# Kernel tuning notes

Measured on AMD Instinct MI355X. Metric: run time of the kernel, lower is better.

## Reference

```python
import jax, jax.numpy as jnp
import numpy as np
import math

DIM = 1024
D_FF = 1024
B = 128


def setup_inputs() -> dict:
    key = jax.random.key(0)
    ks = jax.random.split(key, 13)
    s = 1.0 / math.sqrt(DIM)
    sf = 1.0 / math.sqrt(D_FF)
    return {
        "x": jax.random.normal(ks[0], (B, DIM), dtype=jnp.float32),
        "Wq": jax.random.uniform(ks[1], (DIM, DIM), jnp.float32, -s, s),
        "bq": jax.random.uniform(ks[2], (DIM,), jnp.float32, -s, s),
        "Wk": jax.random.uniform(ks[3], (DIM, DIM), jnp.float32, -s, s),
        "bk": jax.random.uniform(ks[4], (DIM,), jnp.float32, -s, s),
        "Wv": jax.random.uniform(ks[5], (DIM, DIM), jnp.float32, -s, s),
        "bv": jax.random.uniform(ks[6], (DIM,), jnp.float32, -s, s),
        "Wo": jax.random.uniform(ks[7], (DIM, DIM), jnp.float32, -s, s),
        "bo": jax.random.uniform(ks[8], (DIM,), jnp.float32, -s, s),
        "W1": jax.random.uniform(ks[9], (D_FF, DIM), jnp.float32, -s, s),
        "b1": jax.random.uniform(ks[10], (D_FF,), jnp.float32, -s, s),
        "W2": jax.random.uniform(ks[11], (DIM, D_FF), jnp.float32, -sf, sf),
        "b2": jax.random.uniform(ks[12], (DIM,), jnp.float32, -sf, sf),
    }


def reference(x, Wq, bq, Wk, bk, Wv, bv, Wo, bo, W1, b1, W2, b2):
    # Attention (eval mode: dropout is identity)
    q = x @ Wq.T + bq                      # [B, D]
    k = x @ Wk.T + bk                      # [B, D]
    v = x @ Wv.T + bv                      # [B, D]
    inv_sqrt_dk = 1.0 / math.sqrt(DIM)
    # per-sample outer product: weights[b, i, j] = q[b,i] * k[b,j] / sqrt(d_k)
    weights = (q[:, :, None] * k[:, None, :]) * inv_sqrt_dk  # [B, D, D]
    nw = jax.nn.softmax(weights, axis=-1)                    # [B, D, D]
    attn_out = jnp.einsum('bij,bj->bi', nw, v)               # [B, D]
    attn_out = attn_out @ Wo.T + bo
    # residual 1
    x2 = x + attn_out
    # FFN
    h = jax.nn.relu(x2 @ W1.T + b1)        # [B, d_ff]
    ff = h @ W2.T + b2                     # [B, D]
    out = x2 + ff
    return (out, nw)
```

## Files before the change

kernel.cpp:

```cpp
#include <hip/hip_runtime.h>

#define DIM   1024
#define BATCH 128
#define MAT   (BATCH*DIM)
#define NROWS MAT
#define DS    32

typedef float f4n __attribute__((ext_vector_type(4)));

#define A1_R0 0
#define A1_N  26624
#define B1_R0 26624
#define B1_N  17408
#define A2_R0 44032
#define A2_N  26624
#define B2_R0 70656
#define B2_N  17408
#define A3_R0 88064
#define A3_N  26624
#define B3_R0 114688
#define B3_N  16384

struct Params {
  const float *x,*Wq,*bq,*Wk,*bk,*Wv,*bv,*Wo,*bo,*W1,*b1,*W2,*b2;
  float *out,*nw;
  float *q,*k,*v,*araw,*x2,*h,*rinv,*P;
};

__device__ __forceinline__ void fill_write(const Params& p, int T, int NT,
                                           int row0, int nrows)
{
  const size_t base = (size_t)row0 << 8;
  const size_t end  = base + ((size_t)nrows << 8);
  f4n* __restrict__ nw4 = (f4n*)p.nw;
#pragma unroll 2
  for (size_t f = base + T; f < end; f += NT) {
    const int row = (int)(f >> 8);
    const int c4  = (int)(f & 255);
    const int b   = row >> 10;
    const f4n kk = *(const f4n*)(p.k + ((size_t)b<<10) + (c4<<2));
    const float c    = p.q[row] * 0.03125f;
    const float rinv = p.rinv[row];
    f4n st;
    st.x=__expf(c*kk.x)*rinv; st.y=__expf(c*kk.y)*rinv;
    st.z=__expf(c*kk.z)*rinv; st.w=__expf(c*kk.w)*rinv;
    nw4[f] = st;
  }
}

__device__ __forceinline__ void gemm_tile(
    const float* __restrict__ X, const float* __restrict__ W,
    float* __restrict__ Pout, int n0, int k0, int KC,
    float* xt, float* wt)
{
  const int tid = threadIdx.x;
  const int tn = tid & 15, tb = tid >> 4;
  const int b_base = tb*8, n_base = tn*4;
  float acc[8][4];
#pragma unroll
  for (int i=0;i<8;++i)
#pragma unroll
    for (int j=0;j<4;++j) acc[i][j]=0.f;

  for (int s=0; s<KC/DS; ++s) {
    const int kk = k0 + s*DS;
#pragma unroll
    for (int r=0;r<4;++r) {
      const int row = (tid>>3) + 32*r;
      const int c0  = (tid&7)*4;
      const float4 vv = *(const float4*)(X + (size_t)row*DIM + kk + c0);
      xt[(c0+0)*132+row]=vv.x; xt[(c0+1)*132+row]=vv.y;
      xt[(c0+2)*132+row]=vv.z; xt[(c0+3)*132+row]=vv.w;
    }
#pragma unroll
    for (int r=0;r<2;++r) {
      const int row = (tid>>3) + 32*r;
      const int c0  = (tid&7)*4;
      const f4n vv = __builtin_nontemporal_load(
          (const f4n*)(W + (size_t)(n0+row)*DIM + kk + c0));
      wt[(c0+0)*68+row]=vv.x; wt[(c0+1)*68+row]=vv.y;
      wt[(c0+2)*68+row]=vv.z; wt[(c0+3)*68+row]=vv.w;
    }
    __syncthreads();
#pragma unroll 4
    for (int d=0; d<DS; ++d) {
      const float4 xa0 = *(const float4*)&xt[d*132 + b_base];
      const float4 xa1 = *(const float4*)&xt[d*132 + b_base + 4];
      const float4 wa  = *(const float4*)&wt[d*68  + n_base];
      const float xr[8] = {xa0.x,xa0.y,xa0.z,xa0.w, xa1.x,xa1.y,xa1.z,xa1.w};
      const float wr[4] = {wa.x,wa.y,wa.z,wa.w};
#pragma unroll
      for (int bb=0;bb<8;++bb)
#pragma unroll
        for (int nn=0;nn<4;++nn) acc[bb][nn] += xr[bb]*wr[nn];
    }
    __syncthreads();
  }
#pragma unroll
  for (int bb=0;bb<8;++bb) {
    const float4 st = make_float4(acc[bb][0],acc[bb][1],acc[bb][2],acc[bb][3]);
    *(float4*)(Pout + (size_t)(b_base+bb)*DIM + n0 + n_base) = st;
  }
}

__global__ __launch_bounds__(256) void qkv_partial(
    const float* __restrict__ X, const float* __restrict__ W0,
    const float* __restrict__ W1, const float* __restrict__ W2,
    float* __restrict__ P)
{
  __shared__ float xt[DS*132];
  __shared__ float wt[DS*68];
  const int z = blockIdx.z;
  const float* W = (z==0)?W0:(z==1)?W1:W2;
  gemm_tile(X, W, P + (size_t)(z*8+blockIdx.y)*MAT,
            blockIdx.x*64, blockIdx.y*128, 128, xt, wt);
}

__global__ __launch_bounds__(256) void qkv_reduce(Params p)
{
  const int t = blockIdx.x*256 + threadIdx.x;
  const int z = t >> 15, idx4 = t & 32767;
  const float4* Pz = (const float4*)(p.P + (size_t)z*8*MAT);
  const float*  bias = (z==0) ? p.bq : (z==1) ? p.bk : p.bv;
  float* outz = (z==0) ? p.q : (z==1) ? p.k : p.v;
  float4 s = Pz[idx4];
#pragma unroll
  for (int sp=1; sp<8; ++sp) {
    const float4 t2 = Pz[sp*(MAT/4)+idx4];
    s.x+=t2.x; s.y+=t2.y; s.z+=t2.z; s.w+=t2.w;
  }
  const float4 b4 = ((const float4*)bias)[idx4 & 255];
  s.x+=b4.x; s.y+=b4.y; s.z+=b4.z; s.w+=b4.w;
  ((float4*)outz)[idx4] = s;
}

__global__ __launch_bounds__(256,4) void attn_ar(Params p)
{
  const int gw = blockIdx.x*4 + (threadIdx.x>>6);
  const int lane = threadIdx.x & 63;
  const int b = gw >> 5;
  const float4* __restrict__ k4 = (const float4*)(p.k + ((size_t)b<<10));
  const float4* __restrict__ v4 = (const float4*)(p.v + ((size_t)b<<10));
  float4 kr[4], vr[4];
#pragma unroll
  for (int t=0;t<4;++t) { kr[t] = k4[lane + 64*t]; vr[t] = v4[lane + 64*t]; }
  const int r0 = gw*32;
#pragma unroll 1
  for (int r=0;r<32;++r) {
    const int row = r0 + r;
    const float c = p.q[row] * 0.03125f;
    float sum=0.f, dot=0.f;
#pragma unroll
    for (int t=0;t<4;++t) {
      const float ex=__expf(c*kr[t].x), ey=__expf(c*kr[t].y);
      const float ez=__expf(c*kr[t].z), ew=__expf(c*kr[t].w);
      sum += (ex+ey)+(ez+ew);
      dot += ex*vr[t].x + ey*vr[t].y + ez*vr[t].z + ew*vr[t].w;
    }
#pragma unroll
    for (int off=32; off>=1; off>>=1) {
      sum += __shfl_xor(sum, off);
      dot += __shfl_xor(dot, off);
    }
    const float rinv = 1.f/sum;
    if (lane==0) { p.araw[row] = dot*rinv; p.rinv[row] = rinv; }
  }
}

__global__ __launch_bounds__(256,4) void chainA(Params p,
    const float* __restrict__ X, const float* __restrict__ W,
    int row0, int nrows)
{
  __shared__ float xt[DS*132];
  __shared__ float wt[DS*68];
  const int bid = blockIdx.x, tid = threadIdx.x;
  if (bid < 256) {
    gemm_tile(X, W, p.P + (size_t)(bid&15)*MAT, (bid>>4)*64, (bid&15)*64, 64, xt, wt);
  } else {
    fill_write(p, (bid-256)*256 + tid, 768*256, row0, nrows);
  }
}

__global__ __launch_bounds__(256,4) void chainB(Params p,
    const float* __restrict__ bias, const float* __restrict__ extra,
    float* __restrict__ out, int relu, int row0, int nrows)
{
  const int bid = blockIdx.x, tid = threadIdx.x;
  if (bid < 128) {
    const int idx4 = bid*256 + tid;
    const float4* P4 = (const float4*)p.P;
    float4 s = P4[idx4];
#pragma unroll
    for (int sp=1; sp<16; ++sp) {
      const float4 t2 = P4[sp*(MAT/4)+idx4];
      s.x+=t2.x; s.y+=t2.y; s.z+=t2.z; s.w+=t2.w;
    }
    const float4 b4 = ((const float4*)bias)[idx4 & 255];
    s.x+=b4.x; s.y+=b4.y; s.z+=b4.z; s.w+=b4.w;
    if (relu) { s.x=fmaxf(s.x,0.f); s.y=fmaxf(s.y,0.f);
                s.z=fmaxf(s.z,0.f); s.w=fmaxf(s.w,0.f); }
    if (extra) {
      const float4 e = ((const float4*)extra)[idx4];
      s.x+=e.x; s.y+=e.y; s.z+=e.z; s.w+=e.w;
    }
    ((float4*)out)[idx4] = s;
  } else {
    fill_write(p, (bid-128)*256 + tid, 896*256, row0, nrows);
  }
}

extern "C" void kernel_launch(void* const* d_in, const int* in_sizes, int n_in,
                              void* d_out, int out_size, void* d_ws, size_t ws_size,
                              hipStream_t stream)
{
  (void)in_sizes; (void)n_in; (void)out_size; (void)ws_size;
  Params p;
  p.x  = (const float*)d_in[0];
  p.Wq = (const float*)d_in[1];  p.bq = (const float*)d_in[2];
  p.Wk = (const float*)d_in[3];  p.bk = (const float*)d_in[4];
  p.Wv = (const float*)d_in[5];  p.bv = (const float*)d_in[6];
  p.Wo = (const float*)d_in[7];  p.bo = (const float*)d_in[8];
  p.W1 = (const float*)d_in[9];  p.b1 = (const float*)d_in[10];
  p.W2 = (const float*)d_in[11]; p.b2 = (const float*)d_in[12];
  p.out = (float*)d_out;
  p.nw  = p.out + MAT;
  float* ws = (float*)d_ws;
  p.q    = ws;         p.k    = ws + MAT;   p.v = ws + 2*MAT;
  p.araw = ws + 3*MAT; p.x2   = ws + 4*MAT; p.h = ws + 5*MAT;
  p.rinv = ws + 6*MAT; p.P    = ws + 7*MAT;

  qkv_partial<<<dim3(16,8,3), 256, 0, stream>>>(p.x, p.Wq, p.Wk, p.Wv, p.P);
  qkv_reduce<<<384, 256, 0, stream>>>(p);

  attn_ar<<<1024, 256, 0, stream>>>(p);

  chainA<<<1024, 256, 0, stream>>>(p, p.araw, p.Wo, A1_R0, A1_N);
  chainB<<<1024, 256, 0, stream>>>(p, p.bo, p.x, p.x2, 0, B1_R0, B1_N);

  chainA<<<1024, 256, 0, stream>>>(p, p.x2, p.W1, A2_R0, A2_N);
  chainB<<<1024, 256, 0, stream>>>(p, p.b1, nullptr, p.h, 1, B2_R0, B2_N);

  chainA<<<1024, 256, 0, stream>>>(p, p.h, p.W2, A3_R0, A3_N);
  chainB<<<1024, 256, 0, stream>>>(p, p.b2, p.x2, p.out, 0, B3_R0, B3_N);
}
```

Before: 207.5 us.

## Split nw softmax writer out of GEMM chain into dedicated wave-per-row kernel

The large softmax-weights output write was previously interleaved into the GEMM and reduce kernels as extra blocks, so it overlapped with the dependent Wo/W1/W2 chain. The write now runs as a separate kernel after the chain, where each wave holds k in registers and writes whole rows contiguously. The GEMM and reduce kernels launch only the blocks they need. This gives a cleaner, coalesced write stream and smaller launches, but it gives up the overlap of the bandwidth-bound write with the latency-bound GEMM chain.

```diff
diff --git a/kernel.cpp b/kernel.cpp
--- a/kernel.cpp
+++ b/kernel.cpp
@@ -8,45 +8,11 @@
 
 typedef float f4n __attribute__((ext_vector_type(4)));
 
-#define A1_R0 0
-#define A1_N  26624
-#define B1_R0 26624
-#define B1_N  17408
-#define A2_R0 44032
-#define A2_N  26624
-#define B2_R0 70656
-#define B2_N  17408
-#define A3_R0 88064
-#define A3_N  26624
-#define B3_R0 114688
-#define B3_N  16384
-
 struct Params {
   const float *x,*Wq,*bq,*Wk,*bk,*Wv,*bv,*Wo,*bo,*W1,*b1,*W2,*b2;
   float *out,*nw;
   float *q,*k,*v,*araw,*x2,*h,*rinv,*P;
 };
-
-__device__ __forceinline__ void fill_write(const Params& p, int T, int NT,
-                                           int row0, int nrows)
-{
-  const size_t base = (size_t)row0 << 8;
-  const size_t end  = base + ((size_t)nrows << 8);
-  f4n* __restrict__ nw4 = (f4n*)p.nw;
-#pragma unroll 2
-  for (size_t f = base + T; f < end; f += NT) {
-    const int row = (int)(f >> 8);
-    const int c4  = (int)(f & 255);
-    const int b   = row >> 10;
-    const f4n kk = *(const f4n*)(p.k + ((size_t)b<<10) + (c4<<2));
-    const float c    = p.q[row] * 0.03125f;
-    const float rinv = p.rinv[row];
-    f4n st;
-    st.x=__expf(c*kk.x)*rinv; st.y=__expf(c*kk.y)*rinv;
-    st.z=__expf(c*kk.z)*rinv; st.w=__expf(c*kk.w)*rinv;
-    nw4[f] = st;
-  }
-}
 
 __device__ __forceinline__ void gemm_tile(
     const float* __restrict__ X, const float* __restrict__ W,
@@ -167,45 +133,65 @@
   }
 }
 
-__global__ __launch_bounds__(256,4) void chainA(Params p,
-    const float* __restrict__ X, const float* __restrict__ W,
-    int row0, int nrows)
+__global__ __launch_bounds__(256) void gemmA(Params p,
+    const float* __restrict__ X, const float* __restrict__ W)
 {
   __shared__ float xt[DS*132];
   __shared__ float wt[DS*68];
-  const int bid = blockIdx.x, tid = threadIdx.x;
-  if (bid < 256) {
-    gemm_tile(X, W, p.P + (size_t)(bid&15)*MAT, (bid>>4)*64, (bid&15)*64, 64, xt, wt);
-  } else {
-    fill_write(p, (bid-256)*256 + tid, 768*256, row0, nrows);
-  }
-}
-
-__global__ __launch_bounds__(256,4) void chainB(Params p,
+  const int bid = blockIdx.x;
+  gemm_tile(X, W, p.P + (size_t)(bid&15)*MAT, (bid>>4)*64, (bid&15)*64, 64, xt, wt);
+}
+
+__global__ __launch_bounds__(256) void reduceB(Params p,
     const float* __restrict__ bias, const float* __restrict__ extra,
-    float* __restrict__ out, int relu, int row0, int nrows)
-{
-  const int bid = blockIdx.x, tid = threadIdx.x;
-  if (bid < 128) {
-    const int idx4 = bid*256 + tid;
-    const float4* P4 = (const float4*)p.P;
-    float4 s = P4[idx4];
-#pragma unroll
-    for (int sp=1; sp<16; ++sp) {
-      const float4 t2 = P4[sp*(MAT/4)+idx4];
-      s.x+=t2.x; s.y+=t2.y; s.z+=t2.z; s.w+=t2.w;
-    }
-    const float4 b4 = ((const float4*)bias)[idx4 & 255];
-    s.x+=b4.x; s.y+=b4.y; s.z+=b4.z; s.w+=b4.w;
-    if (relu) { s.x=fmaxf(s.x,0.f); s.y=fmaxf(s.y,0.f);
-                s.z=fmaxf(s.z,0.f); s.w=fmaxf(s.w,0.f); }
-    if (extra) {
-      const float4 e = ((const float4*)extra)[idx4];
-      s.x+=e.x; s.y+=e.y; s.z+=e.z; s.w+=e.w;
-    }
-    ((float4*)out)[idx4] = s;
-  } else {
-    fill_write(p, (bid-128)*256 + tid, 896*256, row0, nrows);
+    float* __restrict__ out, int relu)
+{
+  const int idx4 = blockIdx.x*256 + threadIdx.x;
+  const float4* P4 = (const float4*)p.P;
+  float4 s = P4[idx4];
+#pragma unroll
+  for (int sp=1; sp<16; ++sp) {
+    const float4 t2 = P4[sp*(MAT/4)+idx4];
+    s.x+=t2.x; s.y+=t2.y; s.z+=t2.z; s.w+=t2.w;
+  }
+  const float4 b4 = ((const float4*)bias)[idx4 & 255];
+  s.x+=b4.x; s.y+=b4.y; s.z+=b4.z; s.w+=b4.w;
+  if (relu) { s.x=fmaxf(s.x,0.f); s.y=fmaxf(s.y,0.f);
+              s.z=fmaxf(s.z,0.f); s.w=fmaxf(s.w,0.f); }
+  if (extra) {
+    const float4 e = ((const float4*)extra)[idx4];
+    s.x+=e.x; s.y+=e.y; s.z+=e.z; s.w+=e.w;
+  }
+  ((float4*)out)[idx4] = s;
+}
+
+__global__ __launch_bounds__(256,4) void big_writer(Params p)
+{
+  const int g = blockIdx.x*4 + (threadIdx.x>>6);
+  const int lane = threadIdx.x & 63;
+  const int b = g >> 6;
+  const float4* __restrict__ k4 = (const float4*)(p.k + ((size_t)b<<10));
+  const float4 k0 = k4[lane], k1 = k4[lane+64], k2 = k4[lane+128], k3 = k4[lane+192];
+  const int r0 = g*16;
+#pragma unroll 1
+  for (int r=0;r<16;++r) {
+    const int row = r0 + r;
+    const float c    = p.q[row] * 0.03125f;
+    const float rinv = p.rinv[row];
+    float4* o = (float4*)(p.nw + ((size_t)row<<10));
+    float4 s0, s1, s2, s3;
+    s0.x=__expf(c*k0.x)*rinv; s0.y=__expf(c*k0.y)*rinv;
+    s0.z=__expf(c*k0.z)*rinv; s0.w=__expf(c*k0.w)*rinv;
+    s1.x=__expf(c*k1.x)*rinv; s1.y=__expf(c*k1.y)*rinv;
+    s1.z=__expf(c*k1.z)*rinv; s1.w=__expf(c*k1.w)*rinv;
+    s2.x=__expf(c*k2.x)*rinv; s2.y=__expf(c*k2.y)*rinv;
+    s2.z=__expf(c*k2.z)*rinv; s2.w=__expf(c*k2.w)*rinv;
+    s3.x=__expf(c*k3.x)*rinv; s3.y=__expf(c*k3.y)*rinv;
+    s3.z=__expf(c*k3.z)*rinv; s3.w=__expf(c*k3.w)*rinv;
+    o[lane      ] = s0;
+    o[lane +  64] = s1;
+    o[lane + 128] = s2;
+    o[lane + 192] = s3;
   }
 }
 
@@ -234,12 +220,14 @@
 
   attn_ar<<<1024, 256, 0, stream>>>(p);
 
-  chainA<<<1024, 256, 0, stream>>>(p, p.araw, p.Wo, A1_R0, A1_N);
-  chainB<<<1024, 256, 0, stream>>>(p, p.bo, p.x, p.x2, 0, B1_R0, B1_N);
-
-  chainA<<<1024, 256, 0, stream>>>(p, p.x2, p.W1, A2_R0, A2_N);
-  chainB<<<1024, 256, 0, stream>>>(p, p.b1, nullptr, p.h, 1, B2_R0, B2_N);
-
-  chainA<<<1024, 256, 0, stream>>>(p, p.h, p.W2, A3_R0, A3_N);
-  chainB<<<1024, 256, 0, stream>>>(p, p.b2, p.x2, p.out, 0, B3_R0, B3_N);
-}
+  gemmA<<<256, 256, 0, stream>>>(p, p.araw, p.Wo);
+  reduceB<<<128, 256, 0, stream>>>(p, p.bo, p.x, p.x2, 0);
+
+  gemmA<<<256, 256, 0, stream>>>(p, p.x2, p.W1);
+  reduceB<<<128, 256, 0, stream>>>(p, p.b1, nullptr, p.h, 1);
+
+  gemmA<<<256, 256, 0, stream>>>(p, p.h, p.W2);
+  reduceB<<<128, 256, 0, stream>>>(p, p.b2, p.x2, p.out, 0);
+
+  big_writer<<<2048, 256, 0, stream>>>(p);
+}
```

Result: no change. 205.5 us (-1.0%).
